# Optimization experiments

Measured on AMD Instinct MI355X. Metric: run time of the kernel, lower is better.

Reference implementation:

```python
import jax, jax.numpy as jnp
import numpy as np
import math

N, B, D, K = 2000, 2000, 32, 3  # nodes, bills, dim, order+1


def setup_inputs() -> dict:
    key = jax.random.key(0)
    ks = jax.random.split(key, 6)
    return {
        "events": jax.random.randint(ks[0], (N, B), 0, 2) > 0,          # [N,B] bool votes
        "events_time": jax.random.uniform(ks[1], (B,), dtype=jnp.float32),  # [B] bill times
        "beta": jax.random.uniform(ks[2], (B,), dtype=jnp.float32),     # bill bias
        "gamma": jax.random.uniform(ks[3], (N,), dtype=jnp.float32),    # politician bias
        "z_b": jax.random.uniform(ks[4], (B, D), dtype=jnp.float32),    # bill embeddings
        "z_p": jax.random.uniform(ks[5], (K, N, D), dtype=jnp.float32), # stacked order-o politician coeffs
    }


def reference(events, events_time, beta, gamma, z_b, z_p):
    k = z_p.shape[0]
    inv_fact = jnp.asarray([1.0 / math.factorial(o) for o in range(k)], dtype=z_p.dtype)
    # powers[o, b] = t_b**o  (o=0 handled explicitly so grads are safe at t=0)
    powers = jnp.stack(
        [jnp.ones_like(events_time) if o == 0 else events_time ** o for o in range(k)]
    )  # [K,B]
    coeff = powers * inv_fact[:, None]                     # [K,B]  t^o/o!
    pos = jnp.einsum('kb,knd->bnd', coeff, z_p)            # [B,N,D] politician positions at each bill time
    diff = pos - z_b[:, None, :]                           # [B,N,D]
    dist = jnp.sqrt(jnp.sum(diff * diff, axis=-1))         # [B,N] Euclidean distance
    logits = gamma[None, :] + beta[:, None] - dist         # [B,N]
    # log p if voted, log(1-p) otherwise; log(1-sigmoid(x)) == log_sigmoid(-x)
    ll = jnp.where(events.T, jax.nn.log_sigmoid(logits), jax.nn.log_sigmoid(-logits))
    return -jnp.sum(ll)
```

## Files before the change

### kernel.cpp

```cpp
#include <hip/hip_runtime.h>
#include <hip/hip_fp16.h>
#include <math.h>

#define NN    2000
#define NB    2000
#define DD    32
#define PAD   2048
#define NOCT  12
#define TILE  64
#define GDIM  (PAD / TILE)
#define NPART (GDIM * GDIM)

typedef _Float16 half8  __attribute__((ext_vector_type(8)));
typedef float    float4v __attribute__((ext_vector_type(4)));

#define ZF_OFF 0
#define WF_OFF (NOCT * PAD * 8 * 2)
#define BP_OFF (2 * WF_OFF)
#define NP_OFF (BP_OFF + PAD * 16)
#define PT_OFF (NP_OFF + PAD * 8 * 4)

__global__ __launch_bounds__(256) void pol2vec_prep(
    const float* __restrict__ zb, const float* __restrict__ zp,
    const float* __restrict__ gamma, const float* __restrict__ tarr,
    const float* __restrict__ beta,
    _Float16* __restrict__ ZfF, _Float16* __restrict__ WF,
    float4* __restrict__ bp4, float* __restrict__ npar)
{
    const int u = blockIdx.x * 256 + threadIdx.x;
    if (u < NOCT * PAD) {
        const int o = u / PAD, b = u - o * PAD;
        _Float16* dst = ZfF + (size_t)u * 8;
        if (b < NB) {
            const float t = tarr[b];
            const float s = (o < 4) ? 1.f : (o < 8) ? t : 0.5f * t * t;
            const float* zrow = zb + (size_t)b * DD + 8 * (o & 3);
#pragma unroll
            for (int i = 0; i < 8; ++i) dst[i] = (_Float16)(s * zrow[i]);
        } else {
#pragma unroll
            for (int i = 0; i < 8; ++i) dst[i] = (_Float16)0.f;
        }
    } else if (u < 2 * NOCT * PAD) {
        const int u2 = u - NOCT * PAD;
        const int o = u2 / PAD, n = u2 - o * PAD;
        _Float16* dst = WF + (size_t)u2 * 8;
        if (n < NN) {
            const int ksel = o >> 2;
            const float* src = zp + ((size_t)ksel * NN + n) * DD + 8 * (o & 3);
#pragma unroll
            for (int i = 0; i < 8; ++i) dst[i] = (_Float16)src[i];
        } else {
#pragma unroll
            for (int i = 0; i < 8; ++i) dst[i] = (_Float16)0.f;
        }
    } else if (u < 2 * NOCT * PAD + PAD) {
        const int b = u - 2 * NOCT * PAD;
        float4 v = {0.f, 0.f, 0.f, 0.f};
        if (b < NB) {
            float z2 = 0.f;
            const float* zrow = zb + (size_t)b * DD;
#pragma unroll
            for (int d = 0; d < DD; ++d) z2 = fmaf(zrow[d], zrow[d], z2);
            v.x = tarr[b]; v.y = beta[b]; v.z = z2;
        }
        bp4[b] = v;
    } else if (u < 2 * NOCT * PAD + 2 * PAD) {
        const int n = u - 2 * NOCT * PAD - PAD;
        float* o = npar + (size_t)n * 8;
        if (n < NN) {
            const float* pA = zp + (size_t)n * DD;
            const float* pB = zp + ((size_t)NN + n) * DD;
            const float* pC = zp + ((size_t)2 * NN + n) * DD;
            float aa = 0.f, ab = 0.f, ac = 0.f, bb = 0.f, bc = 0.f, cc = 0.f;
#pragma unroll
            for (int d = 0; d < DD; ++d) {
                const float a = pA[d], b = pB[d], c = pC[d];
                aa = fmaf(a, a, aa); ab = fmaf(a, b, ab); ac = fmaf(a, c, ac);
                bb = fmaf(b, b, bb); bc = fmaf(b, c, bc); cc = fmaf(c, c, cc);
            }
            o[0] = aa;         o[1] = 2.f * ab;  o[2] = bb + ac;
            o[3] = bc;         o[4] = 0.25f * cc; o[5] = gamma[n];
            o[6] = 0.f;        o[7] = 0.f;
        } else {
#pragma unroll
            for (int i = 0; i < 8; ++i) o[i] = 0.f;
        }
    }
}

__global__ __launch_bounds__(256, 4) void pol2vec_main(
    const int* __restrict__ events,
    const _Float16* __restrict__ ZfF, const _Float16* __restrict__ WF,
    const float4* __restrict__ bp4, const float* __restrict__ npar,
    float* __restrict__ partials)
{
    __shared__ float4 s_bp[TILE];
    __shared__ float  s_np[TILE][8];
    __shared__ float  s_red[4];

    const int tid  = threadIdx.x;
    const int lane = tid & 63;
    const int w    = tid >> 6;
    const int b0   = blockIdx.x * TILE;
    const int n0   = blockIdx.y * TILE;
    const int wr   = (w >> 1) * 32;
    const int wc   = (w & 1) * 32;
    const int l15  = lane & 15;
    const int l4   = lane >> 4;

    if (tid < TILE) s_bp[tid] = bp4[b0 + tid];
    for (int u = tid; u < TILE * 8; u += 256)
        s_np[u >> 3][u & 7] = npar[((size_t)(n0 + (u >> 3))) * 8 + (u & 7)];

    half8 af[2][3], bf[2][3];
#pragma unroll
    for (int ks = 0; ks < 3; ++ks) {
        const int oct = 4 * ks + l4;
#pragma unroll
        for (int h = 0; h < 2; ++h) {
            af[h][ks] = *(const half8*)(WF  + ((size_t)oct * PAD + (n0 + wr + 16 * h + l15)) * 8);
            bf[h][ks] = *(const half8*)(ZfF + ((size_t)oct * PAD + (b0 + wc + 16 * h + l15)) * 8);
        }
    }

    unsigned evb = 0u, vb = 0u;
#pragma unroll
    for (int nr = 0; nr < 2; ++nr)
#pragma unroll
    for (int bc = 0; bc < 2; ++bc)
#pragma unroll
    for (int r = 0; r < 4; ++r) {
        const int ng = n0 + wr + 16 * nr + l4 * 4 + r;
        const int bg = b0 + wc + 16 * bc + l15;
        const bool v = (ng < NN) && (bg < NB);
        const size_t idx = v ? ((size_t)ng * NB + bg) : 0;
        const unsigned bit = 1u << (nr * 8 + bc * 4 + r);
        if (v) vb |= bit;
        if (v && events[idx]) evb |= bit;
    }

    float4v acc[2][2] = {};
#pragma unroll
    for (int nr = 0; nr < 2; ++nr)
#pragma unroll
    for (int bc = 0; bc < 2; ++bc)
#pragma unroll
    for (int ks = 0; ks < 3; ++ks)
        acc[nr][bc] = __builtin_amdgcn_mfma_f32_16x16x32_f16(
            af[nr][ks], bf[bc][ks], acc[nr][bc], 0, 0, 0);

    __syncthreads();

    float accs = 0.f;
#pragma unroll
    for (int bc = 0; bc < 2; ++bc) {
        const int bl = wc + 16 * bc + l15;
        const float4 bp = s_bp[bl];
        const float t = bp.x, be = bp.y, z2 = bp.z;
#pragma unroll
        for (int nr = 0; nr < 2; ++nr) {
#pragma unroll
            for (int r = 0; r < 4; ++r) {
                const int nl = wr + 16 * nr + l4 * 4 + r;
                const float* cc = s_np[nl];
                const float dot = acc[nr][bc][r];
                const float pv = fmaf(t, fmaf(t, fmaf(t, fmaf(t, cc[4], cc[3]),
                                                      cc[2]), cc[1]), cc[0]);
                const float d2 = fmaxf(fmaf(-2.f, dot, pv + z2), 0.f);
                const float L  = cc[5] + be - sqrtf(d2);
                const unsigned bit = 1u << (nr * 8 + bc * 4 + r);
                const float sgn = (evb & bit) ? 1.f : -1.f;
                const float s   = sgn * L;
                const float term = fmaxf(-s, 0.f) + __logf(1.f + __expf(-fabsf(s)));
                accs += (vb & bit) ? term : 0.f;
            }
        }
    }

#pragma unroll
    for (int o = 32; o > 0; o >>= 1) accs += __shfl_down(accs, o, 64);
    if (lane == 0) s_red[w] = accs;
    __syncthreads();
    if (tid == 0)
        partials[blockIdx.y * GDIM + blockIdx.x] =
            (s_red[0] + s_red[1]) + (s_red[2] + s_red[3]);
}

__global__ __launch_bounds__(256) void pol2vec_reduce(
    const float4* __restrict__ p4, float* __restrict__ out)
{
    __shared__ float s_red[4];
    const int tid = threadIdx.x;
    const float4 v = p4[tid];
    float s = (v.x + v.y) + (v.z + v.w);
#pragma unroll
    for (int o = 32; o > 0; o >>= 1) s += __shfl_down(s, o, 64);
    if ((tid & 63) == 0) s_red[tid >> 6] = s;
    __syncthreads();
    if (tid == 0) out[0] = (s_red[0] + s_red[1]) + (s_red[2] + s_red[3]);
}

extern "C" void kernel_launch(void* const* d_in, const int* in_sizes, int n_in,
                              void* d_out, int out_size, void* d_ws, size_t ws_size,
                              hipStream_t stream) {
    const int*   events = (const int*)d_in[0];
    const float* tarr   = (const float*)d_in[1];
    const float* beta   = (const float*)d_in[2];
    const float* gamma  = (const float*)d_in[3];
    const float* zb     = (const float*)d_in[4];
    const float* zp     = (const float*)d_in[5];
    float* out = (float*)d_out;

    _Float16* ZfF   = (_Float16*)((char*)d_ws + ZF_OFF);
    _Float16* WF    = (_Float16*)((char*)d_ws + WF_OFF);
    float4*  bp4    = (float4*)((char*)d_ws + BP_OFF);
    float*   npar   = (float*)((char*)d_ws + NP_OFF);
    float*   parts  = (float*)((char*)d_ws + PT_OFF);

    const int prep_units = 2 * NOCT * PAD + 2 * PAD;
    pol2vec_prep<<<(prep_units + 255) / 256, 256, 0, stream>>>(
        zb, zp, gamma, tarr, beta, ZfF, WF, bp4, npar);

    dim3 grid(GDIM, GDIM);
    pol2vec_main<<<grid, 256, 0, stream>>>(events, ZfF, WF, bp4, npar, parts);

    pol2vec_reduce<<<1, 256, 0, stream>>>((const float4*)parts, out);
}
```

Measured before the change: 23.44 us.

## Fold squared-norm terms into MFMA K dimension and fuse final reduction

```diff
diff --git a/kernel.cpp b/kernel.cpp
--- a/kernel.cpp
+++ b/kernel.cpp
@@ -6,7 +6,7 @@
 #define NB    2000
 #define DD    32
 #define PAD   2048
-#define NOCT  12
+#define NOCT  16
 #define TILE  64
 #define GDIM  (PAD / TILE)
 #define NPART (GDIM * GDIM)
@@ -16,88 +16,84 @@
 
 #define ZF_OFF 0
 #define WF_OFF (NOCT * PAD * 8 * 2)
-#define BP_OFF (2 * WF_OFF)
-#define NP_OFF (BP_OFF + PAD * 16)
-#define PT_OFF (NP_OFF + PAD * 8 * 4)
+#define PT_OFF (2 * (NOCT * PAD * 8 * 2))
+#define CT_OFF (PT_OFF + NPART * 4)
 
 __global__ __launch_bounds__(256) void pol2vec_prep(
     const float* __restrict__ zb, const float* __restrict__ zp,
-    const float* __restrict__ gamma, const float* __restrict__ tarr,
-    const float* __restrict__ beta,
-    _Float16* __restrict__ ZfF, _Float16* __restrict__ WF,
-    float4* __restrict__ bp4, float* __restrict__ npar)
+    const float* __restrict__ tarr,
+    _Float16* __restrict__ ZfF, _Float16* __restrict__ WF)
 {
     const int u = blockIdx.x * 256 + threadIdx.x;
-    if (u < NOCT * PAD) {
+    const int total = NOCT * PAD;
+    float vals[8] = {0.f, 0.f, 0.f, 0.f, 0.f, 0.f, 0.f, 0.f};
+
+    if (u < total) {
         const int o = u / PAD, b = u - o * PAD;
+        if (b < NB) {
+            if (o < 12) {
+                const float t = tarr[b];
+                const float s = (o < 4) ? 1.f : (o < 8) ? t : 0.5f * t * t;
+                const float* zrow = zb + (size_t)b * DD + 8 * (o & 3);
+#pragma unroll
+                for (int i = 0; i < 8; ++i) vals[i] = s * zrow[i];
+            } else if (o == 12) {
+                const float t = tarr[b];
+                const float* zrow = zb + (size_t)b * DD;
+                float z2 = 0.f;
+#pragma unroll
+                for (int d = 0; d < DD; ++d) z2 = fmaf(zrow[d], zrow[d], z2);
+                const float t2 = t * t;
+                vals[0] = -0.5f;        vals[1] = -0.5f * t;
+                vals[2] = -0.5f * t2;   vals[3] = -0.5f * t2 * t;
+                vals[4] = -0.5f * t2 * t2;
+                vals[5] = -0.5f * z2;
+            }
+        }
         _Float16* dst = ZfF + (size_t)u * 8;
-        if (b < NB) {
-            const float t = tarr[b];
-            const float s = (o < 4) ? 1.f : (o < 8) ? t : 0.5f * t * t;
-            const float* zrow = zb + (size_t)b * DD + 8 * (o & 3);
-#pragma unroll
-            for (int i = 0; i < 8; ++i) dst[i] = (_Float16)(s * zrow[i]);
-        } else {
-#pragma unroll
-            for (int i = 0; i < 8; ++i) dst[i] = (_Float16)0.f;
-        }
-    } else if (u < 2 * NOCT * PAD) {
-        const int u2 = u - NOCT * PAD;
+#pragma unroll
+        for (int i = 0; i < 8; ++i) dst[i] = (_Float16)vals[i];
+    } else if (u < 2 * total) {
+        const int u2 = u - total;
         const int o = u2 / PAD, n = u2 - o * PAD;
+        if (n < NN) {
+            if (o < 12) {
+                const int ksel = o >> 2;
+                const float* src = zp + ((size_t)ksel * NN + n) * DD + 8 * (o & 3);
+#pragma unroll
+                for (int i = 0; i < 8; ++i) vals[i] = src[i];
+            } else if (o == 12) {
+                const float* pA = zp + (size_t)n * DD;
+                const float* pB = zp + ((size_t)NN + n) * DD;
+                const float* pC = zp + ((size_t)2 * NN + n) * DD;
+                float aa = 0.f, ab = 0.f, ac = 0.f, bb = 0.f, bc = 0.f, cc = 0.f;
+#pragma unroll
+                for (int d = 0; d < DD; ++d) {
+                    const float a = pA[d], b = pB[d], c = pC[d];
+                    aa = fmaf(a, a, aa); ab = fmaf(a, b, ab); ac = fmaf(a, c, ac);
+                    bb = fmaf(b, b, bb); bc = fmaf(b, c, bc); cc = fmaf(c, c, cc);
+                }
+                vals[0] = aa;        vals[1] = 2.f * ab;
+                vals[2] = bb + ac;   vals[3] = bc;
+                vals[4] = 0.25f * cc;
+                vals[5] = 1.f;
+            }
+        }
         _Float16* dst = WF + (size_t)u2 * 8;
-        if (n < NN) {
-            const int ksel = o >> 2;
-            const float* src = zp + ((size_t)ksel * NN + n) * DD + 8 * (o & 3);
-#pragma unroll
-            for (int i = 0; i < 8; ++i) dst[i] = (_Float16)src[i];
-        } else {
-#pragma unroll
-            for (int i = 0; i < 8; ++i) dst[i] = (_Float16)0.f;
-        }
-    } else if (u < 2 * NOCT * PAD + PAD) {
-        const int b = u - 2 * NOCT * PAD;
-        float4 v = {0.f, 0.f, 0.f, 0.f};
-        if (b < NB) {
-            float z2 = 0.f;
-            const float* zrow = zb + (size_t)b * DD;
-#pragma unroll
-            for (int d = 0; d < DD; ++d) z2 = fmaf(zrow[d], zrow[d], z2);
-            v.x = tarr[b]; v.y = beta[b]; v.z = z2;
-        }
-        bp4[b] = v;
-    } else if (u < 2 * NOCT * PAD + 2 * PAD) {
-        const int n = u - 2 * NOCT * PAD - PAD;
-        float* o = npar + (size_t)n * 8;
-        if (n < NN) {
-            const float* pA = zp + (size_t)n * DD;
-            const float* pB = zp + ((size_t)NN + n) * DD;
-            const float* pC = zp + ((size_t)2 * NN + n) * DD;
-            float aa = 0.f, ab = 0.f, ac = 0.f, bb = 0.f, bc = 0.f, cc = 0.f;
-#pragma unroll
-            for (int d = 0; d < DD; ++d) {
-                const float a = pA[d], b = pB[d], c = pC[d];
-                aa = fmaf(a, a, aa); ab = fmaf(a, b, ab); ac = fmaf(a, c, ac);
-                bb = fmaf(b, b, bb); bc = fmaf(b, c, bc); cc = fmaf(c, c, cc);
-            }
-            o[0] = aa;         o[1] = 2.f * ab;  o[2] = bb + ac;
-            o[3] = bc;         o[4] = 0.25f * cc; o[5] = gamma[n];
-            o[6] = 0.f;        o[7] = 0.f;
-        } else {
-#pragma unroll
-            for (int i = 0; i < 8; ++i) o[i] = 0.f;
-        }
+#pragma unroll
+        for (int i = 0; i < 8; ++i) dst[i] = (_Float16)vals[i];
     }
 }
 
 __global__ __launch_bounds__(256, 4) void pol2vec_main(
     const int* __restrict__ events,
     const _Float16* __restrict__ ZfF, const _Float16* __restrict__ WF,
-    const float4* __restrict__ bp4, const float* __restrict__ npar,
-    float* __restrict__ partials)
+    const float* __restrict__ gamma, const float* __restrict__ beta,
+    float* __restrict__ partials, unsigned* __restrict__ counter,
+    float* __restrict__ out)
 {
-    __shared__ float4 s_bp[TILE];
-    __shared__ float  s_np[TILE][8];
-    __shared__ float  s_red[4];
+    __shared__ float s_red[4];
+    __shared__ int   s_last;
 
     const int tid  = threadIdx.x;
     const int lane = tid & 63;
@@ -109,13 +105,9 @@
     const int l15  = lane & 15;
     const int l4   = lane >> 4;
 
-    if (tid < TILE) s_bp[tid] = bp4[b0 + tid];
-    for (int u = tid; u < TILE * 8; u += 256)
-        s_np[u >> 3][u & 7] = npar[((size_t)(n0 + (u >> 3))) * 8 + (u & 7)];
-
-    half8 af[2][3], bf[2][3];
-#pragma unroll
-    for (int ks = 0; ks < 3; ++ks) {
+    half8 af[2][4], bf[2][4];
+#pragma unroll
+    for (int ks = 0; ks < 4; ++ks) {
         const int oct = 4 * ks + l4;
 #pragma unroll
         for (int h = 0; h < 2; ++h) {
@@ -146,29 +138,23 @@
 #pragma unroll
     for (int bc = 0; bc < 2; ++bc)
 #pragma unroll
-    for (int ks = 0; ks < 3; ++ks)
+    for (int ks = 0; ks < 4; ++ks)
         acc[nr][bc] = __builtin_amdgcn_mfma_f32_16x16x32_f16(
             af[nr][ks], bf[bc][ks], acc[nr][bc], 0, 0, 0);
 
-    __syncthreads();
-
     float accs = 0.f;
 #pragma unroll
     for (int bc = 0; bc < 2; ++bc) {
-        const int bl = wc + 16 * bc + l15;
-        const float4 bp = s_bp[bl];
-        const float t = bp.x, be = bp.y, z2 = bp.z;
+        const int bg = b0 + wc + 16 * bc + l15;
+        const float be = beta[bg < NB ? bg : 0];
 #pragma unroll
         for (int nr = 0; nr < 2; ++nr) {
 #pragma unroll
             for (int r = 0; r < 4; ++r) {
-                const int nl = wr + 16 * nr + l4 * 4 + r;
-                const float* cc = s_np[nl];
-                const float dot = acc[nr][bc][r];
-                const float pv = fmaf(t, fmaf(t, fmaf(t, fmaf(t, cc[4], cc[3]),
-                                                      cc[2]), cc[1]), cc[0]);
-                const float d2 = fmaxf(fmaf(-2.f, dot, pv + z2), 0.f);
-                const float L  = cc[5] + be - sqrtf(d2);
+                const int ng = n0 + wr + 16 * nr + l4 * 4 + r;
+                const float g = gamma[ng < NN ? ng : 0];
+                const float d2 = fmaxf(-2.f * acc[nr][bc][r], 0.f);
+                const float L  = g + be - sqrtf(d2);
                 const unsigned bit = 1u << (nr * 8 + bc * 4 + r);
                 const float sgn = (evb & bit) ? 1.f : -1.f;
                 const float s   = sgn * L;
@@ -182,23 +168,26 @@
     for (int o = 32; o > 0; o >>= 1) accs += __shfl_down(accs, o, 64);
     if (lane == 0) s_red[w] = accs;
     __syncthreads();
-    if (tid == 0)
+    if (tid == 0) {
         partials[blockIdx.y * GDIM + blockIdx.x] =
             (s_red[0] + s_red[1]) + (s_red[2] + s_red[3]);
-}
-
-__global__ __launch_bounds__(256) void pol2vec_reduce(
-    const float4* __restrict__ p4, float* __restrict__ out)
-{
-    __shared__ float s_red[4];
-    const int tid = threadIdx.x;
-    const float4 v = p4[tid];
-    float s = (v.x + v.y) + (v.z + v.w);
-#pragma unroll
-    for (int o = 32; o > 0; o >>= 1) s += __shfl_down(s, o, 64);
-    if ((tid & 63) == 0) s_red[tid >> 6] = s;
+        __threadfence();
+        const unsigned old = atomicAdd(counter, 1u);
+        s_last = ((old & (NPART - 1u)) == (NPART - 1u)) ? 1 : 0;
+    }
     __syncthreads();
-    if (tid == 0) out[0] = (s_red[0] + s_red[1]) + (s_red[2] + s_red[3]);
+
+    if (s_last) {
+        __threadfence();
+        float s = 0.f;
+        for (int i = tid; i < NPART; i += 256) s += partials[i];
+#pragma unroll
+        for (int o = 32; o > 0; o >>= 1) s += __shfl_down(s, o, 64);
+        if (lane == 0) s_red[w] = s;
+        __syncthreads();
+        if (tid == 0)
+            out[0] = (s_red[0] + s_red[1]) + (s_red[2] + s_red[3]);
+    }
 }
 
 extern "C" void kernel_launch(void* const* d_in, const int* in_sizes, int n_in,
@@ -214,16 +203,13 @@
 
     _Float16* ZfF   = (_Float16*)((char*)d_ws + ZF_OFF);
     _Float16* WF    = (_Float16*)((char*)d_ws + WF_OFF);
-    float4*  bp4    = (float4*)((char*)d_ws + BP_OFF);
-    float*   npar   = (float*)((char*)d_ws + NP_OFF);
-    float*   parts  = (float*)((char*)d_ws + PT_OFF);
-
-    const int prep_units = 2 * NOCT * PAD + 2 * PAD;
-    pol2vec_prep<<<(prep_units + 255) / 256, 256, 0, stream>>>(
-        zb, zp, gamma, tarr, beta, ZfF, WF, bp4, npar);
+    float*    parts = (float*)((char*)d_ws + PT_OFF);
+    unsigned* ctr   = (unsigned*)((char*)d_ws + CT_OFF);
+
+    const int prep_units = 2 * NOCT * PAD;
+    pol2vec_prep<<<prep_units / 256, 256, 0, stream>>>(zb, zp, tarr, ZfF, WF);
 
     dim3 grid(GDIM, GDIM);
-    pol2vec_main<<<grid, 256, 0, stream>>>(events, ZfF, WF, bp4, npar, parts);
-
-    pol2vec_reduce<<<1, 256, 0, stream>>>((const float4*)parts, out);
+    pol2vec_main<<<grid, 256, 0, stream>>>(events, ZfF, WF, gamma, beta,
+                                           parts, ctr, out);
 }
```

New measurement: 38.42 us. +63.9%, slower.

## Fuse preprocessing kernel into main tile kernel using shared-memory staging

Applied to the files above, without the earlier changes.

```diff
diff --git a/kernel.cpp b/kernel.cpp
--- a/kernel.cpp
+++ b/kernel.cpp
@@ -11,93 +11,23 @@
 #define GDIM  (PAD / TILE)
 #define NPART (GDIM * GDIM)
 
-typedef _Float16 half8  __attribute__((ext_vector_type(8)));
+typedef _Float16 half8   __attribute__((ext_vector_type(8)));
 typedef float    float4v __attribute__((ext_vector_type(4)));
 
-#define ZF_OFF 0
-#define WF_OFF (NOCT * PAD * 8 * 2)
-#define BP_OFF (2 * WF_OFF)
-#define NP_OFF (BP_OFF + PAD * 16)
-#define PT_OFF (NP_OFF + PAD * 8 * 4)
-
-__global__ __launch_bounds__(256) void pol2vec_prep(
-    const float* __restrict__ zb, const float* __restrict__ zp,
-    const float* __restrict__ gamma, const float* __restrict__ tarr,
+__global__ __launch_bounds__(256, 4) void pol2vec_main(
+    const int*   __restrict__ events,
+    const float* __restrict__ tarr,
     const float* __restrict__ beta,
-    _Float16* __restrict__ ZfF, _Float16* __restrict__ WF,
-    float4* __restrict__ bp4, float* __restrict__ npar)
+    const float* __restrict__ gamma,
+    const float* __restrict__ zb,
+    const float* __restrict__ zp,
+    float*       __restrict__ partials)
 {
-    const int u = blockIdx.x * 256 + threadIdx.x;
-    if (u < NOCT * PAD) {
-        const int o = u / PAD, b = u - o * PAD;
-        _Float16* dst = ZfF + (size_t)u * 8;
-        if (b < NB) {
-            const float t = tarr[b];
-            const float s = (o < 4) ? 1.f : (o < 8) ? t : 0.5f * t * t;
-            const float* zrow = zb + (size_t)b * DD + 8 * (o & 3);
-#pragma unroll
-            for (int i = 0; i < 8; ++i) dst[i] = (_Float16)(s * zrow[i]);
-        } else {
-#pragma unroll
-            for (int i = 0; i < 8; ++i) dst[i] = (_Float16)0.f;
-        }
-    } else if (u < 2 * NOCT * PAD) {
-        const int u2 = u - NOCT * PAD;
-        const int o = u2 / PAD, n = u2 - o * PAD;
-        _Float16* dst = WF + (size_t)u2 * 8;
-        if (n < NN) {
-            const int ksel = o >> 2;
-            const float* src = zp + ((size_t)ksel * NN + n) * DD + 8 * (o & 3);
-#pragma unroll
-            for (int i = 0; i < 8; ++i) dst[i] = (_Float16)src[i];
-        } else {
-#pragma unroll
-            for (int i = 0; i < 8; ++i) dst[i] = (_Float16)0.f;
-        }
-    } else if (u < 2 * NOCT * PAD + PAD) {
-        const int b = u - 2 * NOCT * PAD;
-        float4 v = {0.f, 0.f, 0.f, 0.f};
-        if (b < NB) {
-            float z2 = 0.f;
-            const float* zrow = zb + (size_t)b * DD;
-#pragma unroll
-            for (int d = 0; d < DD; ++d) z2 = fmaf(zrow[d], zrow[d], z2);
-            v.x = tarr[b]; v.y = beta[b]; v.z = z2;
-        }
-        bp4[b] = v;
-    } else if (u < 2 * NOCT * PAD + 2 * PAD) {
-        const int n = u - 2 * NOCT * PAD - PAD;
-        float* o = npar + (size_t)n * 8;
-        if (n < NN) {
-            const float* pA = zp + (size_t)n * DD;
-            const float* pB = zp + ((size_t)NN + n) * DD;
-            const float* pC = zp + ((size_t)2 * NN + n) * DD;
-            float aa = 0.f, ab = 0.f, ac = 0.f, bb = 0.f, bc = 0.f, cc = 0.f;
-#pragma unroll
-            for (int d = 0; d < DD; ++d) {
-                const float a = pA[d], b = pB[d], c = pC[d];
-                aa = fmaf(a, a, aa); ab = fmaf(a, b, ab); ac = fmaf(a, c, ac);
-                bb = fmaf(b, b, bb); bc = fmaf(b, c, bc); cc = fmaf(c, c, cc);
-            }
-            o[0] = aa;         o[1] = 2.f * ab;  o[2] = bb + ac;
-            o[3] = bc;         o[4] = 0.25f * cc; o[5] = gamma[n];
-            o[6] = 0.f;        o[7] = 0.f;
-        } else {
-#pragma unroll
-            for (int i = 0; i < 8; ++i) o[i] = 0.f;
-        }
-    }
-}
-
-__global__ __launch_bounds__(256, 4) void pol2vec_main(
-    const int* __restrict__ events,
-    const _Float16* __restrict__ ZfF, const _Float16* __restrict__ WF,
-    const float4* __restrict__ bp4, const float* __restrict__ npar,
-    float* __restrict__ partials)
-{
-    __shared__ float4 s_bp[TILE];
-    __shared__ float  s_np[TILE][8];
-    __shared__ float  s_red[4];
+    __shared__ _Float16 sW[NOCT * TILE * 8];
+    __shared__ _Float16 sZ[NOCT * TILE * 8];
+    __shared__ float    sNP[TILE][8];
+    __shared__ float    sBP[TILE][4];
+    __shared__ float    s_red[4];
 
     const int tid  = threadIdx.x;
     const int lane = tid & 63;
@@ -109,21 +39,6 @@
     const int l15  = lane & 15;
     const int l4   = lane >> 4;
 
-    if (tid < TILE) s_bp[tid] = bp4[b0 + tid];
-    for (int u = tid; u < TILE * 8; u += 256)
-        s_np[u >> 3][u & 7] = npar[((size_t)(n0 + (u >> 3))) * 8 + (u & 7)];
-
-    half8 af[2][3], bf[2][3];
-#pragma unroll
-    for (int ks = 0; ks < 3; ++ks) {
-        const int oct = 4 * ks + l4;
-#pragma unroll
-        for (int h = 0; h < 2; ++h) {
-            af[h][ks] = *(const half8*)(WF  + ((size_t)oct * PAD + (n0 + wr + 16 * h + l15)) * 8);
-            bf[h][ks] = *(const half8*)(ZfF + ((size_t)oct * PAD + (b0 + wc + 16 * h + l15)) * 8);
-        }
-    }
-
     unsigned evb = 0u, vb = 0u;
 #pragma unroll
     for (int nr = 0; nr < 2; ++nr)
@@ -140,6 +55,87 @@
         if (v && events[idx]) evb |= bit;
     }
 
+    for (int u = tid; u < NOCT * TILE; u += 256) {
+        const int oct = u >> 6, nl = u & 63;
+        const int n = n0 + nl;
+        half8 hv = {};
+        if (n < NN) {
+            const int ksel = oct >> 2;
+            const float* src = zp + ((size_t)ksel * NN + n) * DD + 8 * (oct & 3);
+            const float4 x = ((const float4*)src)[0];
+            const float4 y = ((const float4*)src)[1];
+            hv[0] = (_Float16)x.x; hv[1] = (_Float16)x.y;
+            hv[2] = (_Float16)x.z; hv[3] = (_Float16)x.w;
+            hv[4] = (_Float16)y.x; hv[5] = (_Float16)y.y;
+            hv[6] = (_Float16)y.z; hv[7] = (_Float16)y.w;
+        }
+        *(half8*)(sW + (size_t)u * 8) = hv;
+    }
+
+    for (int u = tid; u < NOCT * TILE; u += 256) {
+        const int oct = u >> 6, bl = u & 63;
+        const int b = b0 + bl;
+        half8 hv = {};
+        if (b < NB) {
+            const float t = tarr[b];
+            const float s = (oct < 4) ? 1.f : (oct < 8) ? t : 0.5f * t * t;
+            const float* src = zb + (size_t)b * DD + 8 * (oct & 3);
+            const float4 x = ((const float4*)src)[0];
+            const float4 y = ((const float4*)src)[1];
+            hv[0] = (_Float16)(s * x.x); hv[1] = (_Float16)(s * x.y);
+            hv[2] = (_Float16)(s * x.z); hv[3] = (_Float16)(s * x.w);
+            hv[4] = (_Float16)(s * y.x); hv[5] = (_Float16)(s * y.y);
+            hv[6] = (_Float16)(s * y.z); hv[7] = (_Float16)(s * y.w);
+        }
+        *(half8*)(sZ + (size_t)u * 8) = hv;
+    }
+
+    if (tid < TILE) {
+        const int b = b0 + tid;
+        float t = 0.f, be = 0.f, z2 = 0.f;
+        if (b < NB) {
+            t = tarr[b]; be = beta[b];
+            const float* zrow = zb + (size_t)b * DD;
+#pragma unroll
+            for (int d = 0; d < DD; ++d) z2 = fmaf(zrow[d], zrow[d], z2);
+        }
+        sBP[tid][0] = t; sBP[tid][1] = be; sBP[tid][2] = z2; sBP[tid][3] = 0.f;
+    } else if (tid < 2 * TILE) {
+        const int nl = tid - TILE;
+        const int n = n0 + nl;
+        float c[6] = {0.f, 0.f, 0.f, 0.f, 0.f, 0.f};
+        if (n < NN) {
+            const float* pA = zp + (size_t)n * DD;
+            const float* pB = zp + ((size_t)NN + n) * DD;
+            const float* pC = zp + ((size_t)2 * NN + n) * DD;
+            float aa = 0.f, ab = 0.f, ac = 0.f, bb = 0.f, bc = 0.f, cc = 0.f;
+#pragma unroll
+            for (int d = 0; d < DD; ++d) {
+                const float a = pA[d], b = pB[d], cv = pC[d];
+                aa = fmaf(a, a, aa); ab = fmaf(a, b, ab); ac = fmaf(a, cv, ac);
+                bb = fmaf(b, b, bb); bc = fmaf(b, cv, bc); cc = fmaf(cv, cv, cc);
+            }
+            c[0] = aa;          c[1] = 2.f * ab;  c[2] = bb + ac;
+            c[3] = bc;          c[4] = 0.25f * cc; c[5] = gamma[n];
+        }
+#pragma unroll
+        for (int i = 0; i < 6; ++i) sNP[nl][i] = c[i];
+        sNP[nl][6] = 0.f; sNP[nl][7] = 0.f;
+    }
+
+    __syncthreads();
+
+    half8 af[2][3], bf[2][3];
+#pragma unroll
+    for (int ks = 0; ks < 3; ++ks) {
+        const int oct = 4 * ks + l4;
+#pragma unroll
+        for (int h = 0; h < 2; ++h) {
+            af[h][ks] = *(const half8*)(sW + ((size_t)oct * TILE + wr + 16 * h + l15) * 8);
+            bf[h][ks] = *(const half8*)(sZ + ((size_t)oct * TILE + wc + 16 * h + l15) * 8);
+        }
+    }
+
     float4v acc[2][2] = {};
 #pragma unroll
     for (int nr = 0; nr < 2; ++nr)
@@ -150,20 +146,19 @@
         acc[nr][bc] = __builtin_amdgcn_mfma_f32_16x16x32_f16(
             af[nr][ks], bf[bc][ks], acc[nr][bc], 0, 0, 0);
 
-    __syncthreads();
-
     float accs = 0.f;
 #pragma unroll
     for (int bc = 0; bc < 2; ++bc) {
         const int bl = wc + 16 * bc + l15;
-        const float4 bp = s_bp[bl];
-        const float t = bp.x, be = bp.y, z2 = bp.z;
+        const float t  = sBP[bl][0];
+        const float be = sBP[bl][1];
+        const float z2 = sBP[bl][2];
 #pragma unroll
         for (int nr = 0; nr < 2; ++nr) {
 #pragma unroll
             for (int r = 0; r < 4; ++r) {
                 const int nl = wr + 16 * nr + l4 * 4 + r;
-                const float* cc = s_np[nl];
+                const float* cc = sNP[nl];
                 const float dot = acc[nr][bc][r];
                 const float pv = fmaf(t, fmaf(t, fmaf(t, fmaf(t, cc[4], cc[3]),
                                                       cc[2]), cc[1]), cc[0]);
@@ -212,18 +207,10 @@
     const float* zp     = (const float*)d_in[5];
     float* out = (float*)d_out;
 
-    _Float16* ZfF   = (_Float16*)((char*)d_ws + ZF_OFF);
-    _Float16* WF    = (_Float16*)((char*)d_ws + WF_OFF);
-    float4*  bp4    = (float4*)((char*)d_ws + BP_OFF);
-    float*   npar   = (float*)((char*)d_ws + NP_OFF);
-    float*   parts  = (float*)((char*)d_ws + PT_OFF);
-
-    const int prep_units = 2 * NOCT * PAD + 2 * PAD;
-    pol2vec_prep<<<(prep_units + 255) / 256, 256, 0, stream>>>(
-        zb, zp, gamma, tarr, beta, ZfF, WF, bp4, npar);
+    float* parts = (float*)d_ws;
 
     dim3 grid(GDIM, GDIM);
-    pol2vec_main<<<grid, 256, 0, stream>>>(events, ZfF, WF, bp4, npar, parts);
-
+    pol2vec_main<<<grid, 256, 0, stream>>>(events, tarr, beta, gamma, zb, zp,
+                                           parts);
     pol2vec_reduce<<<1, 256, 0, stream>>>((const float4*)parts, out);
 }
```

After: 26.27 us. +12.1%, slower.
